# Kernel tuning notes

Hardware: AMD Instinct MI355X
Metric: run time of the kernel (lower is better)

Reference implementation:

```python
import jax, jax.numpy as jnp
import numpy as np

B, C_IN, IMG = 4, 1, 256
E, P = 800, 4            # embed_size, patch_size
H, DH, M = 8, 64, 64     # heads, dim_head=heads**2, num_landmarks
N = (IMG // P) ** 2      # 4096 tokens
OUT = 256                # output_size
RESK = 33                # lucidrains residual depthwise conv kernel
BN_EPS = 1e-5
LN_EPS = 1e-5
PINV_ITERS = 6


def setup_inputs() -> dict:
    key = jax.random.key(0)
    ks = iter(jax.random.split(key, 32))
    def nrm(shape, s=0.02):
        return jax.random.normal(next(ks), shape, jnp.float32) * s
    inp = {"x": jax.random.normal(next(ks), (B, C_IN, IMG, IMG), jnp.float32)}
    # conv stack: (in, out, kernel); last conv has stride=P, padding=0
    for i, (ci, co, kk) in enumerate([(C_IN, 64, 3), (64, 128, 3), (128, 256, 3), (256, E, P)]):
        inp[f"w{i}"] = nrm((co, ci, kk, kk), 0.05)
        inp[f"b{i}"] = jnp.zeros((co,), jnp.float32)
        inp[f"g{i}"] = jnp.ones((co,), jnp.float32)    # BN gamma
        inp[f"be{i}"] = jnp.zeros((co,), jnp.float32)  # BN beta
        inp[f"mu{i}"] = nrm((co,), 0.1)                # BN running mean
        inp[f"var{i}"] = jax.random.uniform(next(ks), (co,), jnp.float32, 0.5, 1.5)
    inp["qkv_w"] = nrm((E, 3 * H * DH))      # to_qkv (no bias)
    inp["out_w"] = nrm((H * DH, E))          # to_out linear
    inp["out_b"] = jnp.zeros((E,), jnp.float32)
    inp["res_w"] = nrm((H, 1, RESK, 1), 0.05)  # depthwise residual conv over token dim
    inp["ln_g"] = jnp.ones((E,), jnp.float32)
    inp["ln_b"] = jnp.zeros((E,), jnp.float32)
    inp["head_w"] = nrm((E, OUT * OUT // N))   # Linear(800, 16)
    inp["head_b"] = jnp.zeros((OUT * OUT // N,), jnp.float32)
    return inp


def conv2d(x, w, b, stride, pad):
    y = jax.lax.conv_general_dilated(x, w, (stride, stride), [(pad, pad), (pad, pad)],
                                     dimension_numbers=("NCHW", "OIHW", "NCHW"))
    return y + b[None, :, None, None]


def bn(x, g, be, mu, var):
    s = g * jax.lax.rsqrt(var + BN_EPS)  # eval-mode BatchNorm
    return x * s[None, :, None, None] + (be - mu * s)[None, :, None, None]


def moore_penrose_pinv(a, iters=PINV_ITERS):
    I = jnp.eye(a.shape[-1], dtype=a.dtype)
    z = jnp.swapaxes(a, -1, -2) / (jnp.max(jnp.abs(a).sum(-1)) * jnp.max(jnp.abs(a).sum(-2)))
    for _ in range(iters):
        az = a @ z
        z = 0.25 * z @ (13.0 * I - az @ (15.0 * I - az @ (7.0 * I - az)))
    return z


def reference(x, w0, b0, g0, be0, mu0, var0, w1, b1, g1, be1, mu1, var1,
              w2, b2, g2, be2, mu2, var2, w3, b3, g3, be3, mu3, var3,
              qkv_w, out_w, out_b, res_w, ln_g, ln_b, head_w, head_b):
    # ---- PatchEmbedConv ----
    h = x
    blocks = [(w0, b0, g0, be0, mu0, var0, 1, 1), (w1, b1, g1, be1, mu1, var1, 1, 1),
              (w2, b2, g2, be2, mu2, var2, 1, 1), (w3, b3, g3, be3, mu3, var3, P, 0)]
    for w, b, g, be, mu, var, st, pd in blocks:
        h = jax.nn.relu(bn(conv2d(h, w, b, st, pd), g, be, mu, var))
    tok = h.reshape(B, E, N).transpose(0, 2, 1)  # [B, N, E]

    # ---- NystromAttention (n % m == 0, so no front padding needed) ----
    qkv = tok @ qkv_w  # [B, N, 3*H*DH]
    q, k, v = [t.reshape(B, N, H, DH).transpose(0, 2, 1, 3) for t in jnp.split(qkv, 3, axis=-1)]
    q = q * (DH ** -0.5)
    l = N // M
    q_l = q.reshape(B, H, M, l, DH).mean(3)  # landmark means over consecutive blocks
    k_l = k.reshape(B, H, M, l, DH).mean(3)
    a1 = jax.nn.softmax(jnp.einsum("bhnd,bhmd->bhnm", q, k_l), axis=-1)    # [B,H,N,M]
    a2 = jax.nn.softmax(jnp.einsum("bhmd,bhkd->bhmk", q_l, k_l), axis=-1)  # [B,H,M,M]
    a3 = jax.nn.softmax(jnp.einsum("bhmd,bhnd->bhmn", q_l, k), axis=-1)    # [B,H,M,N]
    out = (a1 @ moore_penrose_pinv(a2)) @ (a3 @ v)  # [B,H,N,DH]
    # residual depthwise conv over the token dim of v (groups = heads)
    res = jax.lax.conv_general_dilated(v, res_w, (1, 1), [(RESK // 2, RESK // 2), (0, 0)],
                                       dimension_numbers=("NCHW", "OIHW", "NCHW"),
                                       feature_group_count=H)
    out = out + res
    out = out.transpose(0, 2, 1, 3).reshape(B, N, H * DH)
    out = out @ out_w + out_b  # [B, N, E]

    # ---- LayerNorm ----
    mu_t = out.mean(-1, keepdims=True)
    var_t = out.var(-1, keepdims=True)
    out = (out - mu_t) * jax.lax.rsqrt(var_t + LN_EPS) * ln_g + ln_b

    # ---- reconstruction head ----
    y = jax.nn.sigmoid(out @ head_w + head_b)  # [B, N, OUT*OUT/N]
    return y.reshape(-1, 1, OUT, OUT)
```

## Files before the change

### kernel.cpp

```cpp
#include <hip/hip_runtime.h>

#define DI __device__ __forceinline__

constexpr float BN_EPS_C = 1e-5f;
constexpr float LN_EPS_C = 1e-5f;

typedef _Float16 half8 __attribute__((ext_vector_type(8)));
typedef float f32x4 __attribute__((ext_vector_type(4)));

constexpr size_t B_H0   = 0;
constexpr size_t B_H1   = 8388608;
constexpr size_t B_H2   = 25165824;
constexpr size_t B_Q    = 25165824;
constexpr size_t B_V    = 58720256;
constexpr size_t B_KT   = 75497472;
constexpr size_t B_ATT  = 92274688;
constexpr size_t B_LNB  = 25165824;
constexpr size_t B_TOK  = 159383552;
constexpr size_t B_WP1  = 185597952;
constexpr size_t B_WP2  = 185745408;
constexpr size_t B_WP3  = 186335232;
constexpr size_t B_QKVT = 192888832;
constexpr size_t B_OWT  = 195346432;
constexpr size_t B_QL   = 196165632;
constexpr size_t B_KL   = 196689920;
constexpr size_t B_KLH  = 197214208;
constexpr size_t B_A2   = 197476352;
constexpr size_t B_W2T  = 198524928;
constexpr size_t B_A3V  = 198787072;
constexpr size_t B_SCAL = 199311360;
constexpr size_t B_HWH  = 199311424;

DI float blockReduceSum(float v) {
  #pragma unroll
  for (int o = 32; o; o >>= 1) v += __shfl_xor(v, o);
  __shared__ float red[4];
  int w = threadIdx.x >> 6;
  __syncthreads();
  if ((threadIdx.x & 63) == 0) red[w] = v;
  __syncthreads();
  return red[0] + red[1] + red[2] + red[3];
}

template <int LP, int RP>
DI void mm16v(const float* L, const float* R, int r0, int c0, float reg[4][4]) {
  #pragma unroll
  for (int i = 0; i < 4; ++i)
    #pragma unroll
    for (int j = 0; j < 4; ++j) reg[i][j] = 0.f;
  #pragma unroll 4
  for (int dd = 0; dd < 64; dd += 4) {
    f32x4 l[4], rv[4];
    #pragma unroll
    for (int i = 0; i < 4; ++i)
      l[i] = *reinterpret_cast<const f32x4*>(&L[(size_t)(r0 + i) * LP + dd]);
    #pragma unroll
    for (int u = 0; u < 4; ++u)
      rv[u] = *reinterpret_cast<const f32x4*>(&R[(size_t)(dd + u) * RP + c0]);
    #pragma unroll
    for (int i = 0; i < 4; ++i)
      #pragma unroll
      for (int u = 0; u < 4; ++u)
        #pragma unroll
        for (int j = 0; j < 4; ++j)
          reg[i][j] = fmaf(l[i][u], rv[u][j], reg[i][j]);
  }
}

__global__ void k_pack_all(
    const float* __restrict__ w1, const float* __restrict__ w2c, const float* __restrict__ w3,
    const float* __restrict__ qkvw, const float* __restrict__ outw, const float* __restrict__ headw,
    _Float16* __restrict__ wp1, _Float16* __restrict__ wp2, _Float16* __restrict__ wp3,
    _Float16* __restrict__ qkvT, _Float16* __restrict__ owT, _Float16* __restrict__ hwh,
    float* __restrict__ scal) {
  size_t i = (size_t)blockIdx.x * 256 + threadIdx.x;
  if (i < 73728) {
    int q = i % 9, ci = (i / 9) % 64, co = i / (9 * 64);
    wp1[((size_t)co * 9 + q) * 64 + ci] = (_Float16)w1[i];
  } else if (i < 368640) {
    size_t j = i - 73728;
    int q = j % 9, ci = (j / 9) % 128, co = j / (9 * 128);
    wp2[((size_t)co * 9 + q) * 128 + ci] = (_Float16)w2c[j];
  } else if (i < 3645440) {
    size_t j = i - 368640;
    int q = j % 16, ci = (j / 16) % 256, co = j / (16 * 256);
    wp3[((size_t)co * 16 + q) * 256 + ci] = (_Float16)w3[j];
  } else if (i < 4874240) {
    size_t j = i - 3645440;
    int n = j % 1536, k = j / 1536;
    qkvT[(size_t)n * 800 + k] = (_Float16)qkvw[j];
  } else if (i < 5283840) {
    size_t j = i - 4874240;
    int n = j % 800, k = j / 800;
    owT[(size_t)n * 512 + k] = (_Float16)outw[j];
  } else if (i < 5296640) {
    size_t j = i - 5283840;
    int n = j % 16, k = j / 16;
    hwh[(size_t)n * 800 + k] = (_Float16)headw[j];
  } else if (i < 5296642) {
    scal[i - 5296640] = 0.f;
  }
}

__global__ __launch_bounds__(256) void k_conv0(
    const float* __restrict__ xb, const float* __restrict__ w0, const float* __restrict__ b0,
    const float* __restrict__ g0, const float* __restrict__ be0, const float* __restrict__ mu0,
    const float* __restrict__ var0, _Float16* __restrict__ h0) {
  const int t = threadIdx.x, co = t & 63, xg = t >> 6;
  const int y = blockIdx.x;
  float wreg[9];
  #pragma unroll
  for (int q = 0; q < 9; ++q) wreg[q] = w0[co * 9 + q];
  float s = g0[co] * rsqrtf(var0[co] + BN_EPS_C);
  float sh = fmaf(b0[co] - mu0[co], s, be0[co]);
  for (int xl = 0; xl < 64; ++xl) {
    int xx = xg * 64 + xl;
    float acc = 0.f;
    #pragma unroll
    for (int dy = 0; dy < 3; ++dy) {
      int yy = y + dy - 1;
      if ((unsigned)yy >= 256u) continue;
      #pragma unroll
      for (int dx = 0; dx < 3; ++dx) {
        int xi = xx + dx - 1;
        if ((unsigned)xi >= 256u) continue;
        acc = fmaf(wreg[dy * 3 + dx], xb[yy * 256 + xi], acc);
      }
    }
    float v = fmaxf(fmaf(acc, s, sh), 0.f);
    h0[((size_t)y * 256 + xx) * 64 + co] = (_Float16)v;
  }
}

template <int CI>
__global__ __launch_bounds__(256) void k_convs(
    const _Float16* __restrict__ in, const _Float16* __restrict__ wp,
    const float* __restrict__ bias, const float* __restrict__ g, const float* __restrict__ be,
    const float* __restrict__ mu, const float* __restrict__ var,
    _Float16* __restrict__ out, int CO, int NCT) {
  __shared__ _Float16 Ab[2][128 * 40];
  __shared__ _Float16 Bb[2][128 * 40];
  constexpr int CPQ = CI / 32;
  constexpr int NCK = 9 * CPQ;
  const int t = threadIdx.x;
  const int bid = blockIdx.x;
  const int xcd = bid & 7, slot = bid >> 3;
  const int pj = slot / NCT, cc = slot % NCT;
  const int p = pj * 8 + xcd;
  const int r0 = p * 128, c0 = cc * 128;

  const int ma = t >> 2, kga = t & 3;
  int ry[2], rx[2];
  #pragma unroll
  for (int s = 0; s < 2; ++s) {
    int r = r0 + ma + s * 64;
    ry[s] = r >> 8;
    rx[s] = r & 255;
  }
  const _Float16* baseB[2];
  #pragma unroll
  for (int s = 0; s < 2; ++s)
    baseB[s] = wp + (size_t)(c0 + ma + s * 64) * 9 * CI + kga * 8;
  const int wo = ma * 40 + kga * 8;

  auto loadA = [&](int s, int ck) -> half8 {
    int q = ck / CPQ, coff = (ck % CPQ) * 32;
    int yy = ry[s] + q / 3 - 1;
    int xx = rx[s] + q % 3 - 1;
    half8 a = {};
    if ((unsigned)yy < 256u && (unsigned)xx < 256u)
      a = *reinterpret_cast<const half8*>(in + ((size_t)yy * 256 + xx) * CI + coff + kga * 8);
    return a;
  };

  {
    half8 a0 = loadA(0, 0), a1 = loadA(1, 0);
    half8 b0v = *reinterpret_cast<const half8*>(baseB[0]);
    half8 b1v = *reinterpret_cast<const half8*>(baseB[1]);
    *reinterpret_cast<half8*>(&Ab[0][wo]) = a0;
    *reinterpret_cast<half8*>(&Ab[0][wo + 2560]) = a1;
    *reinterpret_cast<half8*>(&Bb[0][wo]) = b0v;
    *reinterpret_cast<half8*>(&Bb[0][wo + 2560]) = b1v;
  }
  __syncthreads();

  const int w = t >> 6, lo = t & 15, hi = (t >> 4) & 3;
  const int wm = w >> 1, wn = w & 1;
  const int roA = (wm * 64 + lo) * 40 + 8 * hi;
  const int roB = (wn * 64 + lo) * 40 + 8 * hi;
  f32x4 acc[4][4] = {};

  for (int ck = 0; ck < NCK; ++ck) {
    const int cur = ck & 1;
    const bool more = (ck + 1 < NCK);
    half8 rA0, rA1, rB0, rB1;
    if (more) {
      rA0 = loadA(0, ck + 1);
      rA1 = loadA(1, ck + 1);
      rB0 = *reinterpret_cast<const half8*>(baseB[0] + (ck + 1) * 32);
      rB1 = *reinterpret_cast<const half8*>(baseB[1] + (ck + 1) * 32);
    }
    half8 af[4], bf[4];
    #pragma unroll
    for (int mi = 0; mi < 4; ++mi)
      af[mi] = *reinterpret_cast<const half8*>(&Ab[cur][roA + mi * 640]);
    #pragma unroll
    for (int ni = 0; ni < 4; ++ni)
      bf[ni] = *reinterpret_cast<const half8*>(&Bb[cur][roB + ni * 640]);
    #pragma unroll
    for (int mi = 0; mi < 4; ++mi)
      #pragma unroll
      for (int ni = 0; ni < 4; ++ni)
        acc[mi][ni] = __builtin_amdgcn_mfma_f32_16x16x32_f16(af[mi], bf[ni], acc[mi][ni], 0, 0, 0);
    if (more) {
      *reinterpret_cast<half8*>(&Ab[cur ^ 1][wo]) = rA0;
      *reinterpret_cast<half8*>(&Ab[cur ^ 1][wo + 2560]) = rA1;
      *reinterpret_cast<half8*>(&Bb[cur ^ 1][wo]) = rB0;
      *reinterpret_cast<half8*>(&Bb[cur ^ 1][wo + 2560]) = rB1;
    }
    __syncthreads();
  }

  #pragma unroll
  for (int ni = 0; ni < 4; ++ni) {
    int co = c0 + wn * 64 + ni * 16 + lo;
    float s = g[co] * rsqrtf(var[co] + BN_EPS_C);
    float sh = fmaf(bias[co] - mu[co], s, be[co]);
    #pragma unroll
    for (int mi = 0; mi < 4; ++mi)
      #pragma unroll
      for (int rr = 0; rr < 4; ++rr) {
        int row = r0 + wm * 64 + mi * 16 + hi * 4 + rr;
        float v = fmaxf(fmaf(acc[mi][ni][rr], s, sh), 0.f);
        out[(size_t)row * CO + co] = (_Float16)v;
      }
  }
}

__global__ __launch_bounds__(256) void k_c3(
    const _Float16* __restrict__ h2, const _Float16* __restrict__ wp3,
    const float* __restrict__ b3, const float* __restrict__ g3, const float* __restrict__ be3,
    const float* __restrict__ mu3, const float* __restrict__ var3,
    _Float16* __restrict__ tok) {
  __shared__ _Float16 Abuf[2][128 * 40];
  __shared__ _Float16 Bbuf[2][160 * 40];
  const int t = threadIdx.x;
  const int bid = blockIdx.x;
  const int xcd = bid & 7, slot = bid >> 3;
  const int pj = slot / 5, cc = slot % 5;
  const int p = pj * 8 + xcd;
  const int r0 = p * 128, c0 = cc * 160;
  const int img = r0 >> 12;
  const _Float16* h2i = h2 + (size_t)img * 16777216;

  const int ma = t >> 2, kga = t & 3;
  const _Float16* baseA[2];
  #pragma unroll
  for (int s = 0; s < 2; ++s) {
    int m = ma + s * 64;
    int r = r0 + m;
    int py = (r & 4095) >> 6, px = r & 63;
    baseA[s] = h2i + ((size_t)py * 1024 + px * 4) * 256 + kga * 8;
  }
  const _Float16* baseB[3];
  #pragma unroll
  for (int s = 0; s < 3; ++s) {
    int cb = ma + s * 64;
    baseB[s] = wp3 + (size_t)(c0 + (cb < 160 ? cb : 159)) * 4096 + kga * 8;
  }
  const int wo = ma * 40 + kga * 8;

  const int w = t >> 6, lo = t & 15, hi = (t >> 4) & 3;
  const int wm = w >> 1, wn = w & 1;
  const int roA = (wm * 64 + lo) * 40 + 8 * hi;
  const int roB = (wn * 80 + lo) * 40 + 8 * hi;

  f32x4 acc[4][5] = {};

  {
    half8 a0 = *reinterpret_cast<const half8*>(baseA[0]);
    half8 a1 = *reinterpret_cast<const half8*>(baseA[1]);
    half8 b0v = *reinterpret_cast<const half8*>(baseB[0]);
    half8 b1v = *reinterpret_cast<const half8*>(baseB[1]);
    *reinterpret_cast<half8*>(&Abuf[0][wo]) = a0;
    *reinterpret_cast<half8*>(&Abuf[0][wo + 2560]) = a1;
    *reinterpret_cast<half8*>(&Bbuf[0][wo]) = b0v;
    *reinterpret_cast<half8*>(&Bbuf[0][wo + 2560]) = b1v;
    if (t < 128) {
      half8 b2v = *reinterpret_cast<const half8*>(baseB[2]);
      *reinterpret_cast<half8*>(&Bbuf[0][wo + 5120]) = b2v;
    }
  }
  __syncthreads();

  for (int ck = 0; ck < 128; ++ck) {
    const int cur = ck & 1;
    const bool more = (ck + 1 < 128);
    half8 rA0, rA1, rB0, rB1, rB2;
    if (more) {
      const int kn = (ck + 1) << 5;
      const int q = kn >> 8, qk = kn & 255;
      const int aoff = (q >> 2) * 65536 + (q & 3) * 256 + qk;
      rA0 = *reinterpret_cast<const half8*>(baseA[0] + aoff);
      rA1 = *reinterpret_cast<const half8*>(baseA[1] + aoff);
      rB0 = *reinterpret_cast<const half8*>(baseB[0] + kn);
      rB1 = *reinterpret_cast<const half8*>(baseB[1] + kn);
      if (t < 128) rB2 = *reinterpret_cast<const half8*>(baseB[2] + kn);
    }
    half8 af[4], bf[5];
    #pragma unroll
    for (int mi = 0; mi < 4; ++mi)
      af[mi] = *reinterpret_cast<const half8*>(&Abuf[cur][roA + mi * 640]);
    #pragma unroll
    for (int ni = 0; ni < 5; ++ni)
      bf[ni] = *reinterpret_cast<const half8*>(&Bbuf[cur][roB + ni * 640]);
    #pragma unroll
    for (int mi = 0; mi < 4; ++mi)
      #pragma unroll
      for (int ni = 0; ni < 5; ++ni)
        acc[mi][ni] = __builtin_amdgcn_mfma_f32_16x16x32_f16(af[mi], bf[ni], acc[mi][ni], 0, 0, 0);
    if (more) {
      *reinterpret_cast<half8*>(&Abuf[cur ^ 1][wo]) = rA0;
      *reinterpret_cast<half8*>(&Abuf[cur ^ 1][wo + 2560]) = rA1;
      *reinterpret_cast<half8*>(&Bbuf[cur ^ 1][wo]) = rB0;
      *reinterpret_cast<half8*>(&Bbuf[cur ^ 1][wo + 2560]) = rB1;
      if (t < 128) *reinterpret_cast<half8*>(&Bbuf[cur ^ 1][wo + 5120]) = rB2;
    }
    __syncthreads();
  }

  #pragma unroll
  for (int ni = 0; ni < 5; ++ni) {
    int col = c0 + wn * 80 + ni * 16 + lo;
    float s = g3[col] * rsqrtf(var3[col] + BN_EPS_C);
    float sh = fmaf(b3[col] - mu3[col], s, be3[col]);
    #pragma unroll
    for (int mi = 0; mi < 4; ++mi)
      #pragma unroll
      for (int rr = 0; rr < 4; ++rr) {
        int row = r0 + wm * 64 + mi * 16 + hi * 4 + rr;
        float v = fmaxf(fmaf(acc[mi][ni][rr], s, sh), 0.f);
        tok[(size_t)row * 800 + col] = (_Float16)v;
      }
  }
}

__global__ __launch_bounds__(256) void k_qkv_s(
    const _Float16* __restrict__ tok, const _Float16* __restrict__ qkvT,
    _Float16* __restrict__ qx, _Float16* __restrict__ kTg, _Float16* __restrict__ vx,
    float* __restrict__ ql, float* __restrict__ kl, _Float16* __restrict__ klh) {
  __shared__ _Float16 Ab[2][128 * 40];
  __shared__ _Float16 Bb[2][128 * 40];
  const int t = threadIdx.x;
  const int bid = blockIdx.x;
  const int xcd = bid & 7, slot = bid >> 3;
  const int pj = slot / 12, cc = slot % 12;
  const int p = pj * 8 + xcd;
  const int r0 = p * 128, c0 = cc * 128;

  const int ma = t >> 2, kga = t & 3;
  const _Float16* baseA[2];
  const _Float16* baseB[2];
  #pragma unroll
  for (int s = 0; s < 2; ++s) {
    baseA[s] = tok + (size_t)(r0 + ma + s * 64) * 800 + kga * 8;
    baseB[s] = qkvT + (size_t)(c0 + ma + s * 64) * 800 + kga * 8;
  }
  const int wo = ma * 40 + kga * 8;

  {
    half8 a0 = *reinterpret_cast<const half8*>(baseA[0]);
    half8 a1 = *reinterpret_cast<const half8*>(baseA[1]);
    half8 b0v = *reinterpret_cast<const half8*>(baseB[0]);
    half8 b1v = *reinterpret_cast<const half8*>(baseB[1]);
    *reinterpret_cast<half8*>(&Ab[0][wo]) = a0;
    *reinterpret_cast<half8*>(&Ab[0][wo + 2560]) = a1;
    *reinterpret_cast<half8*>(&Bb[0][wo]) = b0v;
    *reinterpret_cast<half8*>(&Bb[0][wo + 2560]) = b1v;
  }
  __syncthreads();

  const int w = t >> 6, lo = t & 15, hi = (t >> 4) & 3;
  const int wm = w >> 1, wn = w & 1;
  const int roA = (wm * 64 + lo) * 40 + 8 * hi;
  const int roB = (wn * 64 + lo) * 40 + 8 * hi;
  f32x4 acc[4][4] = {};

  for (int ck = 0; ck < 25; ++ck) {
    const int cur = ck & 1;
    const bool more = (ck + 1 < 25);
    half8 rA0, rA1, rB0, rB1;
    if (more) {
      const int kn = (ck + 1) * 32;
      rA0 = *reinterpret_cast<const half8*>(baseA[0] + kn);
      rA1 = *reinterpret_cast<const half8*>(baseA[1] + kn);
      rB0 = *reinterpret_cast<const half8*>(baseB[0] + kn);
      rB1 = *reinterpret_cast<const half8*>(baseB[1] + kn);
    }
    half8 af[4], bf[4];
    #pragma unroll
    for (int mi = 0; mi < 4; ++mi)
      af[mi] = *reinterpret_cast<const half8*>(&Ab[cur][roA + mi * 640]);
    #pragma unroll
    for (int ni = 0; ni < 4; ++ni)
      bf[ni] = *reinterpret_cast<const half8*>(&Bb[cur][roB + ni * 640]);
    #pragma unroll
    for (int mi = 0; mi < 4; ++mi)
      #pragma unroll
      for (int ni = 0; ni < 4; ++ni)
        acc[mi][ni] = __builtin_amdgcn_mfma_f32_16x16x32_f16(af[mi], bf[ni], acc[mi][ni], 0, 0, 0);
    if (more) {
      *reinterpret_cast<half8*>(&Ab[cur ^ 1][wo]) = rA0;
      *reinterpret_cast<half8*>(&Ab[cur ^ 1][wo + 2560]) = rA1;
      *reinterpret_cast<half8*>(&Bb[cur ^ 1][wo]) = rB0;
      *reinterpret_cast<half8*>(&Bb[cur ^ 1][wo + 2560]) = rB1;
    }
    __syncthreads();
  }

  const int seg = cc >> 2;
  const int b = r0 >> 12;
  const int m = ((r0 & 4095) >> 6) + wm;
  if (seg == 1) {
    #pragma unroll
    for (int ni = 0; ni < 4; ++ni) {
      int cseg = (cc & 3) * 128 + wn * 64 + ni * 16 + lo;
      int h = cseg >> 6, d = cseg & 63;
      #pragma unroll
      for (int mi = 0; mi < 4; ++mi)
        #pragma unroll
        for (int rr = 0; rr < 4; ++rr) {
          int row = r0 + wm * 64 + mi * 16 + hi * 4 + rr;
          int nn = row & 4095;
          kTg[((size_t)(b * 8 + h) * 64 + d) * 4096 + nn] = (_Float16)acc[mi][ni][rr];
        }
    }
  } else {
    const float scale = (seg == 0) ? 0.125f : 1.0f;
    _Float16* dst = (seg == 0) ? qx : vx;
    #pragma unroll
    for (int ni = 0; ni < 4; ++ni) {
      int cseg = (cc & 3) * 128 + wn * 64 + ni * 16 + lo;
      int h = cseg >> 6, d = cseg & 63;
      #pragma unroll
      for (int mi = 0; mi < 4; ++mi)
        #pragma unroll
        for (int rr = 0; rr < 4; ++rr) {
          int row = r0 + wm * 64 + mi * 16 + hi * 4 + rr;
          int nn = row & 4095;
          dst[((size_t)(b * 8 + h) * 4096 + nn) * 64 + d] = (_Float16)(acc[mi][ni][rr] * scale);
        }
    }
  }
  if (seg <= 1) {
    const float lscale = ((seg == 0) ? 0.125f : 1.0f) * (1.f / 64.f);
    #pragma unroll
    for (int ni = 0; ni < 4; ++ni) {
      float sum = 0.f;
      #pragma unroll
      for (int mi = 0; mi < 4; ++mi)
        #pragma unroll
        for (int rr = 0; rr < 4; ++rr) sum += acc[mi][ni][rr];
      sum += __shfl_xor(sum, 16);
      sum += __shfl_xor(sum, 32);
      if (hi == 0) {
        int cseg = (cc & 3) * 128 + wn * 64 + ni * 16 + lo;
        int h = cseg >> 6, d = cseg & 63;
        int bh = b * 8 + h;
        float lm = sum * lscale;
        if (seg == 0) {
          ql[((size_t)bh * 64 + m) * 64 + d] = lm;
        } else {
          kl[((size_t)bh * 64 + m) * 64 + d] = lm;
          klh[((size_t)bh * 64 + m) * 64 + d] = (_Float16)lm;
        }
      }
    }
  }
}

__global__ __launch_bounds__(256) void k_op_s(
    const _Float16* __restrict__ attb, const _Float16* __restrict__ owT,
    const float* __restrict__ ob, _Float16* __restrict__ lnb) {
  __shared__ _Float16 Abuf[2][128 * 40];
  __shared__ _Float16 Bbuf[2][160 * 40];
  const int t = threadIdx.x;
  const int bid = blockIdx.x;
  const int xcd = bid & 7, slot = bid >> 3;
  const int pj = slot / 5, cc = slot % 5;
  const int p = pj * 8 + xcd;
  const int r0 = p * 128, c0 = cc * 160;

  const int ma = t >> 2, kga = t & 3;
  const _Float16* baseA[2];
  #pragma unroll
  for (int s = 0; s < 2; ++s)
    baseA[s] = attb + (size_t)(r0 + ma + s * 64) * 512 + kga * 8;
  const _Float16* baseB[3];
  #pragma unroll
  for (int s = 0; s < 3; ++s) {
    int cb = ma + s * 64;
    baseB[s] = owT + (size_t)(c0 + (cb < 160 ? cb : 159)) * 512 + kga * 8;
  }
  const int wo = ma * 40 + kga * 8;

  const int w = t >> 6, lo = t & 15, hi = (t >> 4) & 3;
  const int wm = w >> 1, wn = w & 1;
  const int roA = (wm * 64 + lo) * 40 + 8 * hi;
  const int roB = (wn * 80 + lo) * 40 + 8 * hi;

  f32x4 acc[4][5] = {};

  {
    half8 a0 = *reinterpret_cast<const half8*>(baseA[0]);
    half8 a1 = *reinterpret_cast<const half8*>(baseA[1]);
    half8 b0v = *reinterpret_cast<const half8*>(baseB[0]);
    half8 b1v = *reinterpret_cast<const half8*>(baseB[1]);
    *reinterpret_cast<half8*>(&Abuf[0][wo]) = a0;
    *reinterpret_cast<half8*>(&Abuf[0][wo + 2560]) = a1;
    *reinterpret_cast<half8*>(&Bbuf[0][wo]) = b0v;
    *reinterpret_cast<half8*>(&Bbuf[0][wo + 2560]) = b1v;
    if (t < 128) {
      half8 b2v = *reinterpret_cast<const half8*>(baseB[2]);
      *reinterpret_cast<half8*>(&Bbuf[0][wo + 5120]) = b2v;
    }
  }
  __syncthreads();

  for (int ck = 0; ck < 16; ++ck) {
    const int cur = ck & 1;
    const bool more = (ck + 1 < 16);
    half8 rA0, rA1, rB0, rB1, rB2;
    if (more) {
      const int kn = (ck + 1) << 5;
      rA0 = *reinterpret_cast<const half8*>(baseA[0] + kn);
      rA1 = *reinterpret_cast<const half8*>(baseA[1] + kn);
      rB0 = *reinterpret_cast<const half8*>(baseB[0] + kn);
      rB1 = *reinterpret_cast<const half8*>(baseB[1] + kn);
      if (t < 128) rB2 = *reinterpret_cast<const half8*>(baseB[2] + kn);
    }
    half8 af[4], bf[5];
    #pragma unroll
    for (int mi = 0; mi < 4; ++mi)
      af[mi] = *reinterpret_cast<const half8*>(&Abuf[cur][roA + mi * 640]);
    #pragma unroll
    for (int ni = 0; ni < 5; ++ni)
      bf[ni] = *reinterpret_cast<const half8*>(&Bbuf[cur][roB + ni * 640]);
    #pragma unroll
    for (int mi = 0; mi < 4; ++mi)
      #pragma unroll
      for (int ni = 0; ni < 5; ++ni)
        acc[mi][ni] = __builtin_amdgcn_mfma_f32_16x16x32_f16(af[mi], bf[ni], acc[mi][ni], 0, 0, 0);
    if (more) {
      *reinterpret_cast<half8*>(&Abuf[cur ^ 1][wo]) = rA0;
      *reinterpret_cast<half8*>(&Abuf[cur ^ 1][wo + 2560]) = rA1;
      *reinterpret_cast<half8*>(&Bbuf[cur ^ 1][wo]) = rB0;
      *reinterpret_cast<half8*>(&Bbuf[cur ^ 1][wo + 2560]) = rB1;
      if (t < 128) *reinterpret_cast<half8*>(&Bbuf[cur ^ 1][wo + 5120]) = rB2;
    }
    __syncthreads();
  }

  #pragma unroll
  for (int ni = 0; ni < 5; ++ni) {
    int col = c0 + wn * 80 + ni * 16 + lo;
    float bv = ob[col];
    #pragma unroll
    for (int mi = 0; mi < 4; ++mi)
      #pragma unroll
      for (int rr = 0; rr < 4; ++rr) {
        int row = r0 + wm * 64 + mi * 16 + hi * 4 + rr;
        lnb[(size_t)row * 800 + col] = (_Float16)(acc[mi][ni][rr] + bv);
      }
  }
}

__global__ __launch_bounds__(64) void k_a2(
    const float* __restrict__ ql, const float* __restrict__ kl,
    float* __restrict__ a2, float* __restrict__ scal) {
  __shared__ float sp[64 * 65];
  const int bh = blockIdx.x, t = threadIdx.x;
  const float* qr = ql + ((size_t)bh * 64 + t) * 64;
  const float* kb = kl + (size_t)bh * 4096;
  float mx = -1e30f;
  for (int c = 0; c < 64; ++c) {
    float acc = 0.f;
    #pragma unroll 8
    for (int dd = 0; dd < 64; ++dd) acc = fmaf(qr[dd], kb[c * 64 + dd], acc);
    sp[t * 65 + c] = acc;
    mx = fmaxf(mx, acc);
  }
  float sum = 0.f;
  for (int c = 0; c < 64; ++c) {
    float e = expf(sp[t * 65 + c] - mx);
    sp[t * 65 + c] = e;
    sum += e;
  }
  float inv = 1.f / sum;
  float rs = 0.f;
  for (int c = 0; c < 64; ++c) {
    float p = sp[t * 65 + c] * inv;
    sp[t * 65 + c] = p;
    a2[(size_t)bh * 4096 + t * 64 + c] = p;
    rs += p;
  }
  atomicMax(reinterpret_cast<int*>(scal), __float_as_int(rs));
  __syncthreads();
  float cs = 0.f;
  for (int r = 0; r < 64; ++r) cs += sp[r * 65 + t];
  atomicMax(reinterpret_cast<int*>(scal) + 1, __float_as_int(cs));
}

__global__ __launch_bounds__(256) void k_a3v(
    const float* __restrict__ ql, const _Float16* __restrict__ kT,
    const _Float16* __restrict__ vx, float* __restrict__ a3v) {
  __shared__ float sq[64];
  __shared__ float sP[4096];
  __shared__ float red[4];
  __shared__ float red2[4][64];
  const int t = threadIdx.x;
  const int m = blockIdx.x, bh = blockIdx.y;
  if (t < 64) sq[t] = ql[((size_t)bh * 64 + m) * 64 + t];
  __syncthreads();
  const _Float16* kb = kT + (size_t)bh * 262144;
  float sc[16];
  #pragma unroll
  for (int i = 0; i < 16; ++i) sc[i] = 0.f;
  for (int dd = 0; dd < 64; ++dd) {
    float qv = sq[dd];
    const half8* kr = reinterpret_cast<const half8*>(kb + (size_t)dd * 4096 + t * 16);
    half8 k0 = kr[0], k1 = kr[1];
    #pragma unroll
    for (int i = 0; i < 8; ++i) sc[i] = fmaf(qv, (float)k0[i], sc[i]);
    #pragma unroll
    for (int i = 0; i < 8; ++i) sc[8 + i] = fmaf(qv, (float)k1[i], sc[8 + i]);
  }
  float mx = sc[0];
  #pragma unroll
  for (int i = 1; i < 16; ++i) mx = fmaxf(mx, sc[i]);
  #pragma unroll
  for (int o = 32; o; o >>= 1) mx = fmaxf(mx, __shfl_xor(mx, o));
  if ((t & 63) == 0) red[t >> 6] = mx;
  __syncthreads();
  mx = fmaxf(fmaxf(red[0], red[1]), fmaxf(red[2], red[3]));
  __syncthreads();
  float sum = 0.f;
  #pragma unroll
  for (int i = 0; i < 16; ++i) {
    sc[i] = expf(sc[i] - mx);
    sum += sc[i];
  }
  #pragma unroll
  for (int o = 32; o; o >>= 1) sum += __shfl_xor(sum, o);
  if ((t & 63) == 0) red[t >> 6] = sum;
  __syncthreads();
  sum = red[0] + red[1] + red[2] + red[3];
  float inv = 1.f / sum;
  #pragma unroll
  for (int i = 0; i < 16; ++i) sP[t * 16 + i] = sc[i] * inv;
  __syncthreads();
  const int d = t & 63, seg = t >> 6;
  const _Float16* vb = vx + (size_t)bh * 262144;
  float acc = 0.f;
  for (int n = seg * 1024; n < seg * 1024 + 1024; ++n)
    acc = fmaf(sP[n], (float)vb[(size_t)n * 64 + d], acc);
  red2[seg][d] = acc;
  __syncthreads();
  if (seg == 0)
    a3v[((size_t)bh * 64 + m) * 64 + d] = red2[0][d] + red2[1][d] + red2[2][d] + red2[3][d];
}

__global__ __launch_bounds__(256) void k_pinv(
    const float* __restrict__ a2g, const float* __restrict__ scal,
    const float* __restrict__ a3vg, _Float16* __restrict__ w2t) {
  __shared__ float z[64 * 68];
  __shared__ float az[64 * 68];
  __shared__ float tb[64 * 68];
  const int bh = blockIdx.x, t = threadIdx.x;
  const int r0 = (t >> 4) << 2, c0 = (t & 15) << 2;
  const float* ag = a2g + (size_t)bh * 4096;
  const float denom = 1.f / (scal[0] * scal[1]);
  #pragma unroll
  for (int i = 0; i < 4; ++i)
    #pragma unroll
    for (int j = 0; j < 4; ++j)
      z[(r0 + i) * 68 + c0 + j] = ag[(c0 + j) * 64 + r0 + i] * denom;
  __syncthreads();
  float reg[4][4], val[4][4];
  for (int it = 0; it < 6; ++it) {
    mm16v<64, 68>(ag, z, r0, c0, reg);
    #pragma unroll
    for (int i = 0; i < 4; ++i)
      #pragma unroll
      for (int j = 0; j < 4; ++j) az[(r0 + i) * 68 + c0 + j] = reg[i][j];
    __syncthreads();
    mm16v<68, 68>(az, az, r0, c0, reg);
    #pragma unroll
    for (int i = 0; i < 4; ++i)
      #pragma unroll
      for (int j = 0; j < 4; ++j)
        tb[(r0 + i) * 68 + c0 + j] = 7.f * az[(r0 + i) * 68 + c0 + j] - reg[i][j];
    __syncthreads();
    mm16v<68, 68>(az, tb, r0, c0, reg);
    #pragma unroll
    for (int i = 0; i < 4; ++i)
      #pragma unroll
      for (int j = 0; j < 4; ++j)
        val[i][j] = 15.f * az[(r0 + i) * 68 + c0 + j] - reg[i][j];
    __syncthreads();
    #pragma unroll
    for (int i = 0; i < 4; ++i)
      #pragma unroll
      for (int j = 0; j < 4; ++j) tb[(r0 + i) * 68 + c0 + j] = val[i][j];
    __syncthreads();
    mm16v<68, 68>(z, tb, r0, c0, reg);
    #pragma unroll
    for (int i = 0; i < 4; ++i)
      #pragma unroll
      for (int j = 0; j < 4; ++j)
        val[i][j] = 0.25f * (13.f * z[(r0 + i) * 68 + c0 + j] - reg[i][j]);
    __syncthreads();
    #pragma unroll
    for (int i = 0; i < 4; ++i)
      #pragma unroll
      for (int j = 0; j < 4; ++j) z[(r0 + i) * 68 + c0 + j] = val[i][j];
    __syncthreads();
  }
  mm16v<68, 64>(z, a3vg + (size_t)bh * 4096, r0, c0, reg);
  #pragma unroll
  for (int i = 0; i < 4; ++i)
    #pragma unroll
    for (int j = 0; j < 4; ++j)
      w2t[(size_t)bh * 4096 + (c0 + j) * 64 + (r0 + i)] = (_Float16)reg[i][j];
}

__global__ __launch_bounds__(256) void k_combine_m(
    const _Float16* __restrict__ qx, const _Float16* __restrict__ klh,
    const _Float16* __restrict__ w2t, const _Float16* __restrict__ vx,
    const float* __restrict__ rw, _Float16* __restrict__ att) {
  __shared__ _Float16 sP[64 * 72];
  __shared__ _Float16 sVT[64 * 104];
  __shared__ _Float16 sT[64 * 104];
  __shared__ float sR[33];
  const int t = threadIdx.x, w = t >> 6, lo = t & 15, hi = (t >> 4) & 3;
  const int n0 = blockIdx.x * 64;
  const int h = blockIdx.y, b = blockIdx.z, bh = b * 8 + h;
  if (t < 33) sR[t] = rw[h * 33 + t];
  __syncthreads();
  const _Float16* vb = vx + (size_t)bh * 262144;
  #pragma unroll
  for (int u = 0; u < 24; ++u) {
    int e = t + u * 256;
    int r = e >> 6, d = e & 63;
    int nn = n0 - 16 + r;
    sVT[d * 104 + r] = ((unsigned)nn < 4096u) ? vb[(size_t)nn * 64 + d] : (_Float16)0.f;
  }
  #pragma unroll
  for (int u = 0; u < 24; ++u) {
    int e = t + u * 256;
    int r = e % 96, i = e / 96;
    int j = r - i;
    sT[i * 104 + r] = (j >= 0 && j < 33) ? (_Float16)sR[j] : (_Float16)0.f;
  }
  f32x4 sa[4] = {};
  const _Float16* qp = qx + ((size_t)bh * 4096 + n0 + w * 16 + lo) * 64 + 8 * hi;
  const _Float16* klp = klh + (size_t)bh * 4096;
  #pragma unroll
  for (int c = 0; c < 2; ++c) {
    half8 a = *reinterpret_cast<const half8*>(qp + 32 * c);
    #pragma unroll
    for (int ct = 0; ct < 4; ++ct) {
      half8 bf = *reinterpret_cast<const half8*>(klp + (size_t)(ct * 16 + lo) * 64 + 8 * hi + 32 * c);
      sa[ct] = __builtin_amdgcn_mfma_f32_16x16x32_f16(a, bf, sa[ct], 0, 0, 0);
    }
  }
  #pragma unroll
  for (int r = 0; r < 4; ++r) {
    float mx = fmaxf(fmaxf(sa[0][r], sa[1][r]), fmaxf(sa[2][r], sa[3][r]));
    #pragma unroll
    for (int o = 8; o; o >>= 1) mx = fmaxf(mx, __shfl_xor(mx, o));
    float e0 = expf(sa[0][r] - mx), e1 = expf(sa[1][r] - mx);
    float e2 = expf(sa[2][r] - mx), e3 = expf(sa[3][r] - mx);
    float sm = e0 + e1 + e2 + e3;
    #pragma unroll
    for (int o = 8; o; o >>= 1) sm += __shfl_xor(sm, o);
    float inv = 1.f / sm;
    int row = w * 16 + hi * 4 + r;
    sP[row * 72 + lo] = (_Float16)(e0 * inv);
    sP[row * 72 + 16 + lo] = (_Float16)(e1 * inv);
    sP[row * 72 + 32 + lo] = (_Float16)(e2 * inv);
    sP[row * 72 + 48 + lo] = (_Float16)(e3 * inv);
  }
  __syncthreads();
  f32x4 ao[4] = {};
  const _Float16* w2p = w2t + (size_t)bh * 4096;
  #pragma unroll
  for (int c = 0; c < 2; ++c) {
    half8 a = *reinterpret_cast<const half8*>(&sP[(w * 16 + lo) * 72 + 8 * hi + 32 * c]);
    #pragma unroll
    for (int ct = 0; ct < 4; ++ct) {
      half8 bf = *reinterpret_cast<const half8*>(w2p + (size_t)(ct * 16 + lo) * 64 + 8 * hi + 32 * c);
      ao[ct] = __builtin_amdgcn_mfma_f32_16x16x32_f16(a, bf, ao[ct], 0, 0, 0);
    }
  }
  #pragma unroll
  for (int c = 0; c < 3; ++c) {
    half8 a = *reinterpret_cast<const half8*>(&sT[(w * 16 + lo) * 104 + 8 * hi + 32 * c]);
    #pragma unroll
    for (int ct = 0; ct < 4; ++ct) {
      half8 bf = *reinterpret_cast<const half8*>(&sVT[(ct * 16 + lo) * 104 + 8 * hi + 32 * c]);
      ao[ct] = __builtin_amdgcn_mfma_f32_16x16x32_f16(a, bf, ao[ct], 0, 0, 0);
    }
  }
  _Float16* ab = att + ((size_t)b * 4096) * 512 + (size_t)h * 64;
  #pragma unroll
  for (int ct = 0; ct < 4; ++ct)
    #pragma unroll
    for (int r = 0; r < 4; ++r) {
      int n = n0 + w * 16 + hi * 4 + r;
      ab[(size_t)n * 512 + ct * 16 + lo] = (_Float16)ao[ct][r];
    }
}

__global__ __launch_bounds__(256) void k_ln16(
    _Float16* __restrict__ buf, const float* __restrict__ g, const float* __restrict__ bb) {
  const int t = threadIdx.x;
  _Float16* p = buf + (size_t)blockIdx.x * 800;
  float x0 = (float)p[t], x1 = (float)p[t + 256], x2 = (float)p[t + 512];
  float x3 = (t < 32) ? (float)p[t + 768] : 0.f;
  float s = blockReduceSum(x0 + x1 + x2 + x3);
  float mean = s * (1.f / 800.f);
  float d0 = x0 - mean, d1 = x1 - mean, d2 = x2 - mean;
  float d3 = (t < 32) ? x3 - mean : 0.f;
  float s2 = blockReduceSum(d0 * d0 + d1 * d1 + d2 * d2 + d3 * d3);
  float rstd = rsqrtf(s2 * (1.f / 800.f) + LN_EPS_C);
  p[t] = (_Float16)(d0 * rstd * g[t] + bb[t]);
  p[t + 256] = (_Float16)(d1 * rstd * g[t + 256] + bb[t + 256]);
  p[t + 512] = (_Float16)(d2 * rstd * g[t + 512] + bb[t + 512]);
  if (t < 32) p[t + 768] = (_Float16)(d3 * rstd * g[t + 768] + bb[t + 768]);
}

__global__ __launch_bounds__(256) void k_head_m(
    const _Float16* __restrict__ ln, const _Float16* __restrict__ hwh,
    const float* __restrict__ hb, float* __restrict__ out) {
  const int t = threadIdx.x, w = t >> 6, lo = t & 15, hi = (t >> 4) & 3;
  const int row0 = blockIdx.x * 64 + w * 16;
  const _Float16* ap = ln + (size_t)(row0 + lo) * 800 + 8 * hi;
  const _Float16* bp = hwh + (size_t)lo * 800 + 8 * hi;
  f32x4 acc = {};
  #pragma unroll 5
  for (int k = 0; k < 800; k += 32) {
    half8 a = *reinterpret_cast<const half8*>(ap + k);
    half8 b = *reinterpret_cast<const half8*>(bp + k);
    acc = __builtin_amdgcn_mfma_f32_16x16x32_f16(a, b, acc, 0, 0, 0);
  }
  float bv = hb[lo];
  #pragma unroll
  for (int r = 0; r < 4; ++r) {
    int row = row0 + hi * 4 + r;
    out[(size_t)row * 16 + lo] = 1.f / (1.f + expf(-(acc[r] + bv)));
  }
}

extern "C" void kernel_launch(void* const* d_in, const int* in_sizes, int n_in,
                              void* d_out, int out_size, void* d_ws, size_t ws_size,
                              hipStream_t stream) {
  (void)in_sizes; (void)n_in; (void)out_size; (void)ws_size;
  const float* x     = (const float*)d_in[0];
  const float* w0    = (const float*)d_in[1];
  const float* b0    = (const float*)d_in[2];
  const float* g0    = (const float*)d_in[3];
  const float* be0   = (const float*)d_in[4];
  const float* mu0   = (const float*)d_in[5];
  const float* var0  = (const float*)d_in[6];
  const float* w1    = (const float*)d_in[7];
  const float* b1    = (const float*)d_in[8];
  const float* g1    = (const float*)d_in[9];
  const float* be1   = (const float*)d_in[10];
  const float* mu1   = (const float*)d_in[11];
  const float* var1  = (const float*)d_in[12];
  const float* w2c   = (const float*)d_in[13];
  const float* b2    = (const float*)d_in[14];
  const float* g2    = (const float*)d_in[15];
  const float* be2   = (const float*)d_in[16];
  const float* mu2   = (const float*)d_in[17];
  const float* var2  = (const float*)d_in[18];
  const float* w3    = (const float*)d_in[19];
  const float* b3    = (const float*)d_in[20];
  const float* g3    = (const float*)d_in[21];
  const float* be3   = (const float*)d_in[22];
  const float* mu3   = (const float*)d_in[23];
  const float* var3  = (const float*)d_in[24];
  const float* qkvw  = (const float*)d_in[25];
  const float* outw  = (const float*)d_in[26];
  const float* outbv = (const float*)d_in[27];
  const float* resw  = (const float*)d_in[28];
  const float* lng   = (const float*)d_in[29];
  const float* lnbv  = (const float*)d_in[30];
  const float* headw = (const float*)d_in[31];
  const float* headb = (const float*)d_in[32];

  char* wsb = (char*)d_ws;
  _Float16* h0   = (_Float16*)(wsb + B_H0);
  _Float16* h1   = (_Float16*)(wsb + B_H1);
  _Float16* h2   = (_Float16*)(wsb + B_H2);
  _Float16* qb   = (_Float16*)(wsb + B_Q);
  _Float16* vb   = (_Float16*)(wsb + B_V);
  _Float16* kT   = (_Float16*)(wsb + B_KT);
  _Float16* tok  = (_Float16*)(wsb + B_TOK);
  _Float16* attb = (_Float16*)(wsb + B_ATT);
  _Float16* wp1  = (_Float16*)(wsb + B_WP1);
  _Float16* wp2  = (_Float16*)(wsb + B_WP2);
  _Float16* wp3  = (_Float16*)(wsb + B_WP3);
  _Float16* qkvT = (_Float16*)(wsb + B_QKVT);
  _Float16* owT  = (_Float16*)(wsb + B_OWT);
  _Float16* klh  = (_Float16*)(wsb + B_KLH);
  _Float16* w2t  = (_Float16*)(wsb + B_W2T);
  _Float16* hwh  = (_Float16*)(wsb + B_HWH);
  _Float16* lnb16 = (_Float16*)(wsb + B_LNB);
  float* ql   = (float*)(wsb + B_QL);
  float* kl   = (float*)(wsb + B_KL);
  float* a2   = (float*)(wsb + B_A2);
  float* a3v  = (float*)(wsb + B_A3V);
  float* scal = (float*)(wsb + B_SCAL);

  k_pack_all<<<dim3(20691), 256, 0, stream>>>(
      w1, w2c, w3, qkvw, outw, headw, wp1, wp2, wp3, qkvT, owT, hwh, scal);

  for (int img = 0; img < 4; ++img) {
    k_conv0<<<dim3(256), 256, 0, stream>>>(
        x + (size_t)img * 65536, w0, b0, g0, be0, mu0, var0, h0);
    k_convs<64><<<dim3(512), 256, 0, stream>>>(
        h0, wp1, b1, g1, be1, mu1, var1, h1, 128, 1);
    k_convs<128><<<dim3(1024), 256, 0, stream>>>(
        h1, wp2, b2, g2, be2, mu2, var2, h2 + (size_t)img * 16777216, 256, 2);
  }
  k_c3<<<dim3(640), 256, 0, stream>>>(h2, wp3, b3, g3, be3, mu3, var3, tok);
  k_qkv_s<<<dim3(1536), 256, 0, stream>>>(tok, qkvT, qb, kT, vb, ql, kl, klh);
  k_a2<<<dim3(32), 64, 0, stream>>>(ql, kl, a2, scal);
  k_a3v<<<dim3(64, 32), 256, 0, stream>>>(ql, kT, vb, a3v);
  k_pinv<<<dim3(32), 256, 0, stream>>>(a2, scal, a3v, w2t);
  k_combine_m<<<dim3(64, 8, 4), 256, 0, stream>>>(qb, klh, w2t, vb, resw, attb);
  k_op_s<<<dim3(640), 256, 0, stream>>>(attb, owT, outbv, lnb16);
  k_ln16<<<dim3(16384), 256, 0, stream>>>(lnb16, lng, lnbv);
  k_head_m<<<dim3(256), 256, 0, stream>>>(lnb16, hwh, headb, (float*)d_out);
}
```

Baseline: 1.114 ms.

## Split conv0 grid, stage K-transpose stores through LDS, vectorize a3v V loads

Three independent changes. conv0 now runs on a 2D grid with 16 columns per thread instead of 64, which gives four times more blocks for parallelism. The qkv kernel reuses its shared buffer to transpose the K tile, so kT is written with coalesced 16-byte row stores instead of scattered 2-byte stores. The a3v kernel reads V as half8 vectors and reduces across lanes with shuffles, replacing scalar strided loads. The costs are extra LDS traffic and an added barrier in the qkv epilogue.

```diff
diff --git a/kernel.cpp b/kernel.cpp
--- a/kernel.cpp
+++ b/kernel.cpp
@@ -108,13 +108,15 @@
     const float* __restrict__ var0, _Float16* __restrict__ h0) {
   const int t = threadIdx.x, co = t & 63, xg = t >> 6;
   const int y = blockIdx.x;
+  const int x0 = blockIdx.y * 64 + xg * 16;
   float wreg[9];
   #pragma unroll
   for (int q = 0; q < 9; ++q) wreg[q] = w0[co * 9 + q];
   float s = g0[co] * rsqrtf(var0[co] + BN_EPS_C);
   float sh = fmaf(b0[co] - mu0[co], s, be0[co]);
-  for (int xl = 0; xl < 64; ++xl) {
-    int xx = xg * 64 + xl;
+  #pragma unroll 4
+  for (int xl = 0; xl < 16; ++xl) {
+    int xx = x0 + xl;
     float acc = 0.f;
     #pragma unroll
     for (int dy = 0; dy < 3; ++dy) {
@@ -349,8 +351,9 @@
     const _Float16* __restrict__ tok, const _Float16* __restrict__ qkvT,
     _Float16* __restrict__ qx, _Float16* __restrict__ kTg, _Float16* __restrict__ vx,
     float* __restrict__ ql, float* __restrict__ kl, _Float16* __restrict__ klh) {
-  __shared__ _Float16 Ab[2][128 * 40];
-  __shared__ _Float16 Bb[2][128 * 40];
+  __shared__ _Float16 SH[20480];
+  _Float16* AbP = SH;
+  _Float16* BbP = SH + 10240;
   const int t = threadIdx.x;
   const int bid = blockIdx.x;
   const int xcd = bid & 7, slot = bid >> 3;
@@ -373,10 +376,10 @@
     half8 a1 = *reinterpret_cast<const half8*>(baseA[1]);
     half8 b0v = *reinterpret_cast<const half8*>(baseB[0]);
     half8 b1v = *reinterpret_cast<const half8*>(baseB[1]);
-    *reinterpret_cast<half8*>(&Ab[0][wo]) = a0;
-    *reinterpret_cast<half8*>(&Ab[0][wo + 2560]) = a1;
-    *reinterpret_cast<half8*>(&Bb[0][wo]) = b0v;
-    *reinterpret_cast<half8*>(&Bb[0][wo + 2560]) = b1v;
+    *reinterpret_cast<half8*>(&AbP[wo]) = a0;
+    *reinterpret_cast<half8*>(&AbP[wo + 2560]) = a1;
+    *reinterpret_cast<half8*>(&BbP[wo]) = b0v;
+    *reinterpret_cast<half8*>(&BbP[wo + 2560]) = b1v;
   }
   __syncthreads();
 
@@ -400,20 +403,20 @@
     half8 af[4], bf[4];
     #pragma unroll
     for (int mi = 0; mi < 4; ++mi)
-      af[mi] = *reinterpret_cast<const half8*>(&Ab[cur][roA + mi * 640]);
+      af[mi] = *reinterpret_cast<const half8*>(&AbP[cur * 5120 + roA + mi * 640]);
     #pragma unroll
     for (int ni = 0; ni < 4; ++ni)
-      bf[ni] = *reinterpret_cast<const half8*>(&Bb[cur][roB + ni * 640]);
+      bf[ni] = *reinterpret_cast<const half8*>(&BbP[cur * 5120 + roB + ni * 640]);
     #pragma unroll
     for (int mi = 0; mi < 4; ++mi)
       #pragma unroll
       for (int ni = 0; ni < 4; ++ni)
         acc[mi][ni] = __builtin_amdgcn_mfma_f32_16x16x32_f16(af[mi], bf[ni], acc[mi][ni], 0, 0, 0);
     if (more) {
-      *reinterpret_cast<half8*>(&Ab[cur ^ 1][wo]) = rA0;
-      *reinterpret_cast<half8*>(&Ab[cur ^ 1][wo + 2560]) = rA1;
-      *reinterpret_cast<half8*>(&Bb[cur ^ 1][wo]) = rB0;
-      *reinterpret_cast<half8*>(&Bb[cur ^ 1][wo + 2560]) = rB1;
+      *reinterpret_cast<half8*>(&AbP[(cur ^ 1) * 5120 + wo]) = rA0;
+      *reinterpret_cast<half8*>(&AbP[(cur ^ 1) * 5120 + wo + 2560]) = rA1;
+      *reinterpret_cast<half8*>(&BbP[(cur ^ 1) * 5120 + wo]) = rB0;
+      *reinterpret_cast<half8*>(&BbP[(cur ^ 1) * 5120 + wo + 2560]) = rB1;
     }
     __syncthreads();
   }
@@ -424,16 +427,23 @@
   if (seg == 1) {
     #pragma unroll
     for (int ni = 0; ni < 4; ++ni) {
-      int cseg = (cc & 3) * 128 + wn * 64 + ni * 16 + lo;
-      int h = cseg >> 6, d = cseg & 63;
+      int cl = wn * 64 + ni * 16 + lo;
       #pragma unroll
       for (int mi = 0; mi < 4; ++mi)
         #pragma unroll
         for (int rr = 0; rr < 4; ++rr) {
-          int row = r0 + wm * 64 + mi * 16 + hi * 4 + rr;
-          int nn = row & 4095;
-          kTg[((size_t)(b * 8 + h) * 64 + d) * 4096 + nn] = (_Float16)acc[mi][ni][rr];
+          int nl = wm * 64 + mi * 16 + hi * 4 + rr;
+          SH[cl * 136 + nl] = (_Float16)acc[mi][ni][rr];
         }
+    }
+    __syncthreads();
+    const int base_row = b * 512 + (cc & 3) * 128;
+    const int base_n = (p & 31) * 128;
+    #pragma unroll
+    for (int e = t; e < 2048; e += 256) {
+      int cl = e >> 4, ch = e & 15;
+      half8 vvv = *reinterpret_cast<const half8*>(&SH[cl * 136 + ch * 8]);
+      *reinterpret_cast<half8*>(&kTg[(size_t)(base_row + cl) * 4096 + base_n + ch * 8]) = vvv;
     }
   } else {
     const float scale = (seg == 0) ? 0.125f : 1.0f;
@@ -659,15 +669,28 @@
   #pragma unroll
   for (int i = 0; i < 16; ++i) sP[t * 16 + i] = sc[i] * inv;
   __syncthreads();
-  const int d = t & 63, seg = t >> 6;
+  const int seg = t >> 6, l = t & 63;
+  const int nl = l >> 3, dblk = (l & 7) * 8;
   const _Float16* vb = vx + (size_t)bh * 262144;
-  float acc = 0.f;
-  for (int n = seg * 1024; n < seg * 1024 + 1024; ++n)
-    acc = fmaf(sP[n], (float)vb[(size_t)n * 64 + d], acc);
-  red2[seg][d] = acc;
+  float acc8[8] = {};
+  for (int it = 0; it < 128; ++it) {
+    int n8 = seg * 1024 + it * 8;
+    half8 vv = *reinterpret_cast<const half8*>(&vb[(size_t)(n8 + nl) * 64 + dblk]);
+    float pc = sP[n8 + nl];
+    #pragma unroll
+    for (int u = 0; u < 8; ++u) acc8[u] = fmaf(pc, (float)vv[u], acc8[u]);
+  }
+  #pragma unroll
+  for (int off = 8; off <= 32; off <<= 1)
+    #pragma unroll
+    for (int u = 0; u < 8; ++u) acc8[u] += __shfl_xor(acc8[u], off);
+  if (nl == 0) {
+    #pragma unroll
+    for (int u = 0; u < 8; ++u) red2[seg][dblk + u] = acc8[u];
+  }
   __syncthreads();
   if (seg == 0)
-    a3v[((size_t)bh * 64 + m) * 64 + d] = red2[0][d] + red2[1][d] + red2[2][d] + red2[3][d];
+    a3v[((size_t)bh * 64 + m) * 64 + l] = red2[0][l] + red2[1][l] + red2[2][l] + red2[3][l];
 }
 
 __global__ __launch_bounds__(256) void k_pinv(
@@ -928,7 +951,7 @@
       w1, w2c, w3, qkvw, outw, headw, wp1, wp2, wp3, qkvT, owT, hwh, scal);
 
   for (int img = 0; img < 4; ++img) {
-    k_conv0<<<dim3(256), 256, 0, stream>>>(
+    k_conv0<<<dim3(256, 4), 256, 0, stream>>>(
         x + (size_t)img * 65536, w0, b0, g0, be0, mu0, var0, h0);
     k_convs<64><<<dim3(512), 256, 0, stream>>>(
         h0, wp1, b1, g1, be1, mu1, var1, h1, 128, 1);
```

Measured after the change: 947.8 us. 14.9% less time.
